# Kernel optimization log

Measured on AMD Instinct MI355X. Metric: run time of the kernel, lower is better.

## Reference

```python
import jax, jax.numpy as jnp
import numpy as np

NUM_HEADS = 16
DIM = 1024
HEAD_DIM = DIM // NUM_HEADS
SCALE = DIM ** (-0.5)  # note: module scales by dim_out**-0.5, not head_dim**-0.5
ROPE_THETA = 10000.0


def _rope_cos_sin(seq_len, head_dim, dtype):
    # lucidrains default: freqs = 1/theta^(arange(0,d,2)/d), interleaved-repeat to d
    inv_freq = 1.0 / (ROPE_THETA ** (np.arange(0, head_dim, 2, dtype=np.float32) / head_dim))
    t = np.arange(seq_len, dtype=np.float32)
    freqs = np.einsum('i,j->ij', t, inv_freq)            # [T, d/2]
    freqs = np.repeat(freqs, 2, axis=-1)                  # [T, d] interleaved repeat
    return jnp.asarray(np.cos(freqs), dtype), jnp.asarray(np.sin(freqs), dtype)


def _rotate_half(x):
    # interleaved pairs: (x1, x2) -> (-x2, x1)
    x1 = x[..., ::2]
    x2 = x[..., 1::2]
    return jnp.stack([-x2, x1], axis=-1).reshape(x.shape)


def _apply_rope(x, cos, sin):
    # x: [B, H, T, d]; cos/sin: [T, d]
    return x * cos + _rotate_half(x) * sin


def setup_inputs() -> dict:
    key = jax.random.key(0)
    ks = jax.random.split(key, 6)
    B, T = 4, 2048
    s = DIM ** -0.5
    return {
        'x':  jax.random.normal(ks[0], (B, T, DIM), jnp.float32),
        'h':  32,
        'w':  64,
        'Wq': jax.random.normal(ks[1], (DIM, DIM), jnp.float32) * s,
        'Wk': jax.random.normal(ks[2], (DIM, DIM), jnp.float32) * s,
        'Wv': jax.random.normal(ks[3], (DIM, DIM), jnp.float32) * s,
        'Wp': jax.random.normal(ks[4], (DIM, DIM), jnp.float32) * s,
        'bp': jax.random.normal(ks[5], (DIM,), jnp.float32) * 0.01,
    }


def reference(x, h, w, Wq, Wk, Wv, Wp, bp):
    B, T, _ = x.shape
    split = lambda y: y.reshape(B, T, NUM_HEADS, HEAD_DIM).transpose(0, 2, 1, 3)  # b h t d
    q = split(x @ Wq)
    k = split(x @ Wk)
    v = split(x @ Wv)
    cos, sin = _rope_cos_sin(T, HEAD_DIM, x.dtype)
    q = _apply_rope(q, cos, sin)
    k = _apply_rope(k, cos, sin)
    attn = jax.nn.softmax(jnp.einsum('bhld,bhtd->bhlt', q, k) * SCALE, axis=-1)
    out = jnp.einsum('bhlt,bhtd->bhld', attn, v)
    out = out.transpose(0, 2, 1, 3).reshape(B, T, DIM)  # b t (h d)
    return out @ Wp + bp
```

## Files before the change

kernel.cpp:

```cpp
#include <hip/hip_runtime.h>

typedef unsigned short u16;
typedef unsigned int u32;
typedef __attribute__((ext_vector_type(8))) short short8;
typedef __attribute__((ext_vector_type(4))) short short4v;
typedef __attribute__((ext_vector_type(4))) float f32x4;
typedef __attribute__((ext_vector_type(16))) float f32x16;

__device__ __forceinline__ u16 f2bf(float f) {
  u32 u = __float_as_uint(f);
  u = (u + 0x7fffu + ((u >> 16) & 1u)) >> 16;
  return (u16)u;
}
__device__ __forceinline__ float bf2f(u16 h) {
  return __uint_as_float(((u32)h) << 16);
}
__device__ __forceinline__ void glds16(const u16* g, u16* l) {
  __builtin_amdgcn_global_load_lds(
      (const __attribute__((address_space(1))) void*)g,
      (__attribute__((address_space(3))) void*)l, 16, 0, 0);
}

__global__ __launch_bounds__(256) void rope_tab_k(float* __restrict__ cosT,
                                                  float* __restrict__ sinT) {
  int idx = blockIdx.x * 256 + threadIdx.x;
  int t = idx >> 5, i = idx & 31;
  float inv = powf(10000.0f, -(float)i / 32.0f);
  float ang = (float)t * inv;
  float s, c;
  sincosf(ang, &s, &c);
  cosT[idx] = c;
  sinT[idx] = s;
}

__global__ __launch_bounds__(256) void cvt_x_k(const float* __restrict__ x,
                                               u16* __restrict__ xb) {
  int i = blockIdx.x * 256 + threadIdx.x;
  int e = i * 8;
  float4 a = *(const float4*)(x + e);
  float4 b = *(const float4*)(x + e + 4);
  short8 o;
  o[0] = (short)f2bf(a.x); o[1] = (short)f2bf(a.y);
  o[2] = (short)f2bf(a.z); o[3] = (short)f2bf(a.w);
  o[4] = (short)f2bf(b.x); o[5] = (short)f2bf(b.y);
  o[6] = (short)f2bf(b.z); o[7] = (short)f2bf(b.w);
  *(short8*)(xb + e) = o;
}

__global__ __launch_bounds__(256) void wtrans_k(const float* __restrict__ W0,
                                                const float* __restrict__ W1,
                                                const float* __restrict__ W2,
                                                const float* __restrict__ W3,
                                                u16* __restrict__ wt) {
  __shared__ float tl[64][65];
  const float* W = (blockIdx.z == 0) ? W0 : (blockIdx.z == 1) ? W1
                  : (blockIdx.z == 2) ? W2 : W3;
  u16* out = wt + (size_t)blockIdx.z * 1024 * 1024;
  int k0 = blockIdx.x * 64, n0 = blockIdx.y * 64;
  int tid = threadIdx.x;
  int rr = tid >> 4, cc4 = (tid & 15) * 4;
#pragma unroll
  for (int p = 0; p < 4; ++p) {
    int r = rr + p * 16;
    float4 v = *(const float4*)(W + (size_t)(k0 + r) * 1024 + n0 + cc4);
    tl[r][cc4] = v.x; tl[r][cc4 + 1] = v.y; tl[r][cc4 + 2] = v.z; tl[r][cc4 + 3] = v.w;
  }
  __syncthreads();
#pragma unroll
  for (int p = 0; p < 4; ++p) {
    int rn = rr + p * 16;
    short4v o;
    o[0] = (short)f2bf(tl[cc4][rn]);     o[1] = (short)f2bf(tl[cc4 + 1][rn]);
    o[2] = (short)f2bf(tl[cc4 + 2][rn]); o[3] = (short)f2bf(tl[cc4 + 3][rn]);
    *(short4v*)(out + (size_t)(n0 + rn) * 1024 + k0 + cc4) = o;
  }
}

__global__ __launch_bounds__(256) void gemm_qkv_k(const u16* __restrict__ xb,
                                                  const u16* __restrict__ wt,
                                                  u16* __restrict__ Qb,
                                                  u16* __restrict__ Kb,
                                                  u16* __restrict__ Vt) {
  __shared__ __align__(16) u16 Ash[128][32];
  __shared__ __align__(16) u16 Bsh[128][32];
  int tid = threadIdx.x;
  int lane = tid & 63, w = tid >> 6;
  int wr = w >> 1, wc = w & 1;
  int l15 = lane & 15, g = lane >> 4;
  int row0 = blockIdx.x * 128;
  int ncol0 = blockIdx.y * 128;

  f32x4 zero = {0.f, 0.f, 0.f, 0.f};
  f32x4 acc[4][4];
#pragma unroll
  for (int m = 0; m < 4; ++m)
#pragma unroll
    for (int n = 0; n < 4; ++n) acc[m][n] = zero;

  int aRow = tid >> 2, aK = (tid & 3) * 8;
  const u16* aSrc0 = xb + (size_t)(row0 + aRow) * 1024 + aK;
  const u16* aSrc1 = xb + (size_t)(row0 + 64 + aRow) * 1024 + aK;
  const u16* bSrc0 = wt + (size_t)(ncol0 + aRow) * 1024 + aK;
  const u16* bSrc1 = wt + (size_t)(ncol0 + 64 + aRow) * 1024 + aK;
  u16* ldsA0 = &Ash[0][0] + tid * 8;
  u16* ldsA1 = &Ash[0][0] + 2048 + tid * 8;
  u16* ldsB0 = &Bsh[0][0] + tid * 8;
  u16* ldsB1 = &Bsh[0][0] + 2048 + tid * 8;

  for (int kt = 0; kt < 32; ++kt) {
    __syncthreads();
    glds16(aSrc0, ldsA0); glds16(aSrc1, ldsA1);
    glds16(bSrc0, ldsB0); glds16(bSrc1, ldsB1);
    aSrc0 += 32; aSrc1 += 32; bSrc0 += 32; bSrc1 += 32;
    __syncthreads();
    short8 af[4], bfr[4];
#pragma unroll
    for (int m = 0; m < 4; ++m) af[m] = *(const short8*)&Ash[wr * 64 + m * 16 + l15][g * 8];
#pragma unroll
    for (int n = 0; n < 4; ++n) bfr[n] = *(const short8*)&Bsh[wc * 64 + n * 16 + l15][g * 8];
#pragma unroll
    for (int m = 0; m < 4; ++m)
#pragma unroll
      for (int n = 0; n < 4; ++n)
        acc[m][n] = __builtin_amdgcn_mfma_f32_16x16x32_bf16(af[m], bfr[n], acc[m][n], 0, 0, 0);
  }

  int c0 = ncol0 + wc * 64;
  int which = c0 >> 10;
  int rb = row0 + wr * 64;
#pragma unroll
  for (int m = 0; m < 4; ++m) {
    int r = rb + m * 16 + g * 4;
    int bb = r >> 11, t = r & 2047;
#pragma unroll
    for (int n = 0; n < 4; ++n) {
      int c = c0 + n * 16 + l15;
      int hh = (c & 1023) >> 6, d = c & 63;
      if (which == 2) {
        short4v o;
        o[0] = (short)f2bf(acc[m][n][0]); o[1] = (short)f2bf(acc[m][n][1]);
        o[2] = (short)f2bf(acc[m][n][2]); o[3] = (short)f2bf(acc[m][n][3]);
        *(short4v*)(Vt + ((size_t)((bb * 16 + hh) * 64 + d)) * 2048 + t) = o;
      } else {
        u16* dst = (which == 0 ? Qb : Kb) + ((size_t)((bb * 16 + hh) * 2048 + t)) * 64 + d;
        dst[0]   = f2bf(acc[m][n][0]);
        dst[64]  = f2bf(acc[m][n][1]);
        dst[128] = f2bf(acc[m][n][2]);
        dst[192] = f2bf(acc[m][n][3]);
      }
    }
  }
}

__global__ __launch_bounds__(256) void rope_k(u16* __restrict__ Qb, u16* __restrict__ Kb,
                                              const float* __restrict__ cosT,
                                              const float* __restrict__ sinT) {
  int i = blockIdx.x * 256 + threadIdx.x;
  u16* P; float sc; int j;
  if (i < 1048576) { P = Qb; sc = 0.03125f; j = i; }
  else             { P = Kb; sc = 1.0f;     j = i - 1048576; }
  int e = j * 8;
  int d0 = e & 63;
  int t = (e >> 6) & 2047;
  short8 v = *(const short8*)(P + e);
  const float* cb = cosT + t * 32 + (d0 >> 1);
  const float* sb = sinT + t * 32 + (d0 >> 1);
  short8 o;
#pragma unroll
  for (int p = 0; p < 4; ++p) {
    float c = cb[p], s = sb[p];
    float a = bf2f((u16)v[2 * p]), b = bf2f((u16)v[2 * p + 1]);
    o[2 * p]     = (short)f2bf((a * c - b * s) * sc);
    o[2 * p + 1] = (short)f2bf((b * c + a * s) * sc);
  }
  *(short8*)(P + e) = o;
}

__global__ __launch_bounds__(256) void attn_k(const u16* __restrict__ Q,
                                              const u16* __restrict__ K,
                                              const u16* __restrict__ Vt,
                                              u16* __restrict__ O) {
  __shared__ __align__(16) u16 KVs[2][2][4096];
  int bid = blockIdx.x;
  int head = (bid & 7) + ((bid >> 7) << 3);
  int qt = (bid >> 3) & 15;
  int bb = head >> 4, hh = head & 15;
  const u16* Qh = Q + (size_t)head * 131072;
  const u16* Kh = K + (size_t)head * 131072;
  const u16* Vh = Vt + (size_t)head * 131072;
  int tid = threadIdx.x, lane = tid & 63, w = tid >> 6;
  int l31 = lane & 31, hi = lane >> 5;
  int t0 = qt * 128 + w * 32;

  int srow = tid >> 3;
  int scol = ((tid & 7) ^ (srow & 7)) * 8;

  short8 qf[4];
#pragma unroll
  for (int ks = 0; ks < 4; ++ks)
    qf[ks] = *(const short8*)(Qh + (size_t)(t0 + l31) * 64 + ks * 16 + hi * 8);

  const u16* lds0 = &KVs[0][0][0];
  const u16* rpp[4];
#pragma unroll
  for (int j = 0; j < 4; ++j)
    rpp[j] = lds0 + l31 * 64 + ((((j * 2 + hi) ^ (lane & 7))) << 3);

  f32x16 zz;
#pragma unroll
  for (int i = 0; i < 16; ++i) zz[i] = 0.f;
  f32x16 oa0 = zz, oa1 = zz, oa2 = zz;
  short8 ones8 = {16256, 16256, 16256, 16256, 16256, 16256, 16256, 16256};

  const u16* kp = Kh + srow * 64 + scol;
  const u16* vp = Vh + srow * 2048 + scol;
  u16* sK = &KVs[0][0][0] + tid * 8;
  u16* sV = &KVs[0][1][0] + tid * 8;

#define STAGE_AT(BO) do {                                                      \
    glds16(kp,         sK + (BO));                                             \
    glds16(kp + 2048,  sK + (BO) + 2048);                                      \
    glds16(vp,         sV + (BO));                                             \
    glds16(vp + 65536, sV + (BO) + 2048);                                      \
    kp += 4096; vp += 64;                                                      \
  } while (0)

#define ATT_TILE(OB) do {                                                      \
    _Pragma("unroll")                                                          \
    for (int bl = 0; bl < 2; ++bl) {                                           \
      f32x16 pb = zz;                                                          \
      __builtin_amdgcn_s_setprio(1);                                           \
      _Pragma("unroll")                                                        \
      for (int ks = 0; ks < 4; ++ks) {                                         \
        short8 kf = *(const short8*)(rpp[ks] + (OB) + bl * 2048);              \
        pb = __builtin_amdgcn_mfma_f32_32x32x16_bf16(kf, qf[ks], pb, 0, 0, 0); \
      }                                                                        \
      __builtin_amdgcn_s_setprio(0);                                           \
      _Pragma("unroll")                                                        \
      for (int r = 0; r < 16; ++r) pb[r] = __expf(pb[r]);                      \
      u32 pk8[8];                                                              \
      _Pragma("unroll")                                                        \
      for (int j = 0; j < 8; ++j)                                              \
        asm("v_cvt_pk_bf16_f32 %0, %1, %2"                                     \
            : "=v"(pk8[j]) : "v"(pb[2 * j]), "v"(pb[2 * j + 1]));              \
      _Pragma("unroll")                                                        \
      for (int kb = 0; kb < 2; ++kb) {                                         \
        u32 w0 = pk8[4 * kb + 0], w2 = pk8[4 * kb + 2];                        \
        u32 w1 = pk8[4 * kb + 1], w3 = pk8[4 * kb + 3];                        \
        asm("v_permlane32_swap_b32 %0, %1" : "+v"(w0), "+v"(w2));              \
        asm("v_permlane32_swap_b32 %0, %1" : "+v"(w1), "+v"(w3));              \
        union { u32 u[4]; short8 s; } pu;                                      \
        pu.u[0] = w0; pu.u[1] = w1; pu.u[2] = w2; pu.u[3] = w3;                \
        const int kss = bl * 2 + kb;                                           \
        short8 vf0 = *(const short8*)(rpp[kss] + (OB) + 4096);                 \
        short8 vf1 = *(const short8*)(rpp[kss] + (OB) + 4096 + 2048);          \
        __builtin_amdgcn_s_setprio(1);                                         \
        oa0 = __builtin_amdgcn_mfma_f32_32x32x16_bf16(pu.s, vf0, oa0, 0,0,0);  \
        oa1 = __builtin_amdgcn_mfma_f32_32x32x16_bf16(pu.s, vf1, oa1, 0,0,0);  \
        oa2 = __builtin_amdgcn_mfma_f32_32x32x16_bf16(pu.s, ones8, oa2, 0,0,0);\
        __builtin_amdgcn_s_setprio(0);                                         \
      }                                                                        \
    }                                                                          \
  } while (0)

  STAGE_AT(0);
  for (int it = 0; it < 16; ++it) {
    STAGE_AT(8192);
    asm volatile("s_waitcnt vmcnt(4)\ns_barrier" ::: "memory");
    ATT_TILE(0);
    asm volatile("s_barrier" ::: "memory");
    if (it < 15) {
      STAGE_AT(0);
      asm volatile("s_waitcnt vmcnt(4)\ns_barrier" ::: "memory");
    } else {
      asm volatile("s_waitcnt vmcnt(0)\ns_barrier" ::: "memory");
    }
    ATT_TILE(8192);
    asm volatile("s_barrier" ::: "memory");
  }
#undef STAGE_AT
#undef ATT_TILE

  size_t obase = (size_t)(bb * 2048 + t0) * 1024 + hh * 64 + l31;
#pragma unroll
  for (int r = 0; r < 16; ++r) {
    int qr = (r & 3) + ((r >> 2) << 3) + (hi << 2);
    float ir = 1.0f / oa2[r];
    O[obase + (size_t)qr * 1024]      = f2bf(oa0[r] * ir);
    O[obase + (size_t)qr * 1024 + 32] = f2bf(oa1[r] * ir);
  }
}

__global__ __launch_bounds__(256) void gemm_out_k(const u16* __restrict__ Ob,
                                                  const u16* __restrict__ wt,
                                                  const float* __restrict__ bp,
                                                  float* __restrict__ out) {
  __shared__ __align__(16) u16 Ash[128][32];
  __shared__ __align__(16) u16 Bsh[128][32];
  int tid = threadIdx.x;
  int lane = tid & 63, w = tid >> 6;
  int wr = w >> 1, wc = w & 1;
  int l15 = lane & 15, g = lane >> 4;
  int row0 = blockIdx.x * 128;
  int ncol0 = blockIdx.y * 128;

  f32x4 zero = {0.f, 0.f, 0.f, 0.f};
  f32x4 acc[4][4];
#pragma unroll
  for (int m = 0; m < 4; ++m)
#pragma unroll
    for (int n = 0; n < 4; ++n) acc[m][n] = zero;

  int aRow = tid >> 2, aK = (tid & 3) * 8;
  const u16* aSrc0 = Ob + (size_t)(row0 + aRow) * 1024 + aK;
  const u16* aSrc1 = Ob + (size_t)(row0 + 64 + aRow) * 1024 + aK;
  const u16* bSrc0 = wt + (size_t)(ncol0 + aRow) * 1024 + aK;
  const u16* bSrc1 = wt + (size_t)(ncol0 + 64 + aRow) * 1024 + aK;
  u16* ldsA0 = &Ash[0][0] + tid * 8;
  u16* ldsA1 = &Ash[0][0] + 2048 + tid * 8;
  u16* ldsB0 = &Bsh[0][0] + tid * 8;
  u16* ldsB1 = &Bsh[0][0] + 2048 + tid * 8;

  for (int kt = 0; kt < 32; ++kt) {
    __syncthreads();
    glds16(aSrc0, ldsA0); glds16(aSrc1, ldsA1);
    glds16(bSrc0, ldsB0); glds16(bSrc1, ldsB1);
    aSrc0 += 32; aSrc1 += 32; bSrc0 += 32; bSrc1 += 32;
    __syncthreads();
    short8 af[4], bfr[4];
#pragma unroll
    for (int m = 0; m < 4; ++m) af[m] = *(const short8*)&Ash[wr * 64 + m * 16 + l15][g * 8];
#pragma unroll
    for (int n = 0; n < 4; ++n) bfr[n] = *(const short8*)&Bsh[wc * 64 + n * 16 + l15][g * 8];
#pragma unroll
    for (int m = 0; m < 4; ++m)
#pragma unroll
      for (int n = 0; n < 4; ++n)
        acc[m][n] = __builtin_amdgcn_mfma_f32_16x16x32_bf16(af[m], bfr[n], acc[m][n], 0, 0, 0);
  }

  int c0 = ncol0 + wc * 64;
  int rb = row0 + wr * 64;
  float bn[4];
#pragma unroll
  for (int n = 0; n < 4; ++n) bn[n] = bp[c0 + n * 16 + l15];
#pragma unroll
  for (int m = 0; m < 4; ++m) {
    int r = rb + m * 16 + g * 4;
#pragma unroll
    for (int n = 0; n < 4; ++n) {
      int c = c0 + n * 16 + l15;
      out[(size_t)(r + 0) * 1024 + c] = acc[m][n][0] + bn[n];
      out[(size_t)(r + 1) * 1024 + c] = acc[m][n][1] + bn[n];
      out[(size_t)(r + 2) * 1024 + c] = acc[m][n][2] + bn[n];
      out[(size_t)(r + 3) * 1024 + c] = acc[m][n][3] + bn[n];
    }
  }
}

extern "C" void kernel_launch(void* const* d_in, const int* in_sizes, int n_in,
                              void* d_out, int out_size, void* d_ws, size_t ws_size,
                              hipStream_t stream) {
  const float* x  = (const float*)d_in[0];
  const float* Wq = (const float*)d_in[3];
  const float* Wk = (const float*)d_in[4];
  const float* Wv = (const float*)d_in[5];
  const float* Wp = (const float*)d_in[6];
  const float* bp = (const float*)d_in[7];
  float* out = (float*)d_out;

  char* ws = (char*)d_ws;
  u16* xb   = (u16*)(ws);
  u16* wt   = (u16*)(ws + 16777216);
  u16* Qb   = (u16*)(ws + 25165824);
  u16* Kb   = (u16*)(ws + 41943040);
  u16* Vt   = (u16*)(ws + 58720256);
  u16* Ob   = (u16*)(ws + 75497472);
  float* cosT = (float*)(ws + 92274688);
  float* sinT = (float*)(ws + 92536832);

  rope_tab_k<<<256, 256, 0, stream>>>(cosT, sinT);
  cvt_x_k<<<4096, 256, 0, stream>>>(x, xb);
  dim3 tg(16, 16, 4);
  wtrans_k<<<tg, 256, 0, stream>>>(Wq, Wk, Wv, Wp, wt);
  dim3 g1(64, 24);
  gemm_qkv_k<<<g1, 256, 0, stream>>>(xb, wt, Qb, Kb, Vt);
  rope_k<<<8192, 256, 0, stream>>>(Qb, Kb, cosT, sinT);
  attn_k<<<1024, 256, 0, stream>>>(Qb, Kb, Vt, Ob);
  dim3 g2(64, 8);
  gemm_out_k<<<g2, 256, 0, stream>>>(Ob, wt + (size_t)3 * 1024 * 1024, bp, out);
}
```

Measured before the change: 208.8 us.

## Fuse RoPE into QKV GEMM epilogue and swizzle GEMM block order

The separate rope_k pass over Q and K is removed. RoPE rotation and the Q scale are now applied in the QKV GEMM epilogue, using a packed bf16 cos/sin table staged into LDS and a lane-xor shuffle to get the pair partner. Both GEMMs also remap block indices so that consecutive blocks share tiles, which should improve L2 reuse. In exchange the QKV kernel uses 16KB more LDS, and cos/sin are rounded to bf16, which slightly lowers precision.

```diff
diff --git a/kernel.cpp b/kernel.cpp
--- a/kernel.cpp
+++ b/kernel.cpp
@@ -21,16 +21,14 @@
       (__attribute__((address_space(3))) void*)l, 16, 0, 0);
 }
 
-__global__ __launch_bounds__(256) void rope_tab_k(float* __restrict__ cosT,
-                                                  float* __restrict__ sinT) {
+__global__ __launch_bounds__(256) void rope_tab_k(u32* __restrict__ cst) {
   int idx = blockIdx.x * 256 + threadIdx.x;
   int t = idx >> 5, i = idx & 31;
   float inv = powf(10000.0f, -(float)i / 32.0f);
   float ang = (float)t * inv;
   float s, c;
   sincosf(ang, &s, &c);
-  cosT[idx] = c;
-  sinT[idx] = s;
+  cst[idx] = (u32)f2bf(c) | ((u32)f2bf(s) << 16);
 }
 
 __global__ __launch_bounds__(256) void cvt_x_k(const float* __restrict__ x,
@@ -78,17 +76,31 @@
 
 __global__ __launch_bounds__(256) void gemm_qkv_k(const u16* __restrict__ xb,
                                                   const u16* __restrict__ wt,
+                                                  const u32* __restrict__ cst,
                                                   u16* __restrict__ Qb,
                                                   u16* __restrict__ Kb,
                                                   u16* __restrict__ Vt) {
   __shared__ __align__(16) u16 Ash[128][32];
   __shared__ __align__(16) u16 Bsh[128][32];
+  __shared__ __align__(16) u32 csl[4096];
   int tid = threadIdx.x;
   int lane = tid & 63, w = tid >> 6;
   int wr = w >> 1, wc = w & 1;
   int l15 = lane & 15, g = lane >> 4;
-  int row0 = blockIdx.x * 128;
-  int ncol0 = blockIdx.y * 128;
+
+  int lin = blockIdx.x + blockIdx.y * 64;
+  int sw = (lin & 7) * 192 + (lin >> 3);
+  int bx = sw & 63, by = sw >> 6;
+  int row0 = bx * 128;
+  int ncol0 = by * 128;
+  int which = by >> 3;
+
+  if (which < 2) {
+    const u16* src = (const u16*)(cst + (size_t)(row0 & 2047) * 32);
+#pragma unroll
+    for (int p = 0; p < 4; ++p)
+      glds16(src + p * 2048 + tid * 8, (u16*)csl + p * 2048 + tid * 8);
+  }
 
   f32x4 zero = {0.f, 0.f, 0.f, 0.f};
   f32x4 acc[4][4];
@@ -126,12 +138,14 @@
   }
 
   int c0 = ncol0 + wc * 64;
-  int which = c0 >> 10;
   int rb = row0 + wr * 64;
+  u32 sgnbit = (l15 & 1) ? 0u : 0x80000000u;
+  float qscale = (which == 0) ? 0.03125f : 1.0f;
 #pragma unroll
   for (int m = 0; m < 4; ++m) {
     int r = rb + m * 16 + g * 4;
     int bb = r >> 11, t = r & 2047;
+    int rowin = wr * 64 + m * 16 + g * 4;
 #pragma unroll
     for (int n = 0; n < 4; ++n) {
       int c = c0 + n * 16 + l15;
@@ -143,37 +157,21 @@
         *(short4v*)(Vt + ((size_t)((bb * 16 + hh) * 64 + d)) * 2048 + t) = o;
       } else {
         u16* dst = (which == 0 ? Qb : Kb) + ((size_t)((bb * 16 + hh) * 2048 + t)) * 64 + d;
-        dst[0]   = f2bf(acc[m][n][0]);
-        dst[64]  = f2bf(acc[m][n][1]);
-        dst[128] = f2bf(acc[m][n][2]);
-        dst[192] = f2bf(acc[m][n][3]);
+        int ci = (d >> 1);
+#pragma unroll
+        for (int j = 0; j < 4; ++j) {
+          float v = acc[m][n][j];
+          float p = __shfl_xor(v, 1);
+          u32 cs = csl[(rowin + j) * 32 + ci];
+          float c_ = __uint_as_float(cs << 16);
+          float s_ = __uint_as_float(cs & 0xffff0000u);
+          float ps = __uint_as_float(__float_as_uint(p * s_) ^ sgnbit);
+          float o = fmaf(v, c_, ps) * qscale;
+          dst[j * 64] = f2bf(o);
+        }
       }
     }
   }
-}
-
-__global__ __launch_bounds__(256) void rope_k(u16* __restrict__ Qb, u16* __restrict__ Kb,
-                                              const float* __restrict__ cosT,
-                                              const float* __restrict__ sinT) {
-  int i = blockIdx.x * 256 + threadIdx.x;
-  u16* P; float sc; int j;
-  if (i < 1048576) { P = Qb; sc = 0.03125f; j = i; }
-  else             { P = Kb; sc = 1.0f;     j = i - 1048576; }
-  int e = j * 8;
-  int d0 = e & 63;
-  int t = (e >> 6) & 2047;
-  short8 v = *(const short8*)(P + e);
-  const float* cb = cosT + t * 32 + (d0 >> 1);
-  const float* sb = sinT + t * 32 + (d0 >> 1);
-  short8 o;
-#pragma unroll
-  for (int p = 0; p < 4; ++p) {
-    float c = cb[p], s = sb[p];
-    float a = bf2f((u16)v[2 * p]), b = bf2f((u16)v[2 * p + 1]);
-    o[2 * p]     = (short)f2bf((a * c - b * s) * sc);
-    o[2 * p + 1] = (short)f2bf((b * c + a * s) * sc);
-  }
-  *(short8*)(P + e) = o;
 }
 
 __global__ __launch_bounds__(256) void attn_k(const u16* __restrict__ Q,
@@ -301,8 +299,12 @@
   int lane = tid & 63, w = tid >> 6;
   int wr = w >> 1, wc = w & 1;
   int l15 = lane & 15, g = lane >> 4;
-  int row0 = blockIdx.x * 128;
-  int ncol0 = blockIdx.y * 128;
+
+  int lin = blockIdx.x + blockIdx.y * 64;
+  int sw = (lin & 7) * 64 + (lin >> 3);
+  int bx = sw & 63, by = sw >> 6;
+  int row0 = bx * 128;
+  int ncol0 = by * 128;
 
   f32x4 zero = {0.f, 0.f, 0.f, 0.f};
   f32x4 acc[4][4];
@@ -376,16 +378,14 @@
   u16* Kb   = (u16*)(ws + 41943040);
   u16* Vt   = (u16*)(ws + 58720256);
   u16* Ob   = (u16*)(ws + 75497472);
-  float* cosT = (float*)(ws + 92274688);
-  float* sinT = (float*)(ws + 92536832);
-
-  rope_tab_k<<<256, 256, 0, stream>>>(cosT, sinT);
+  u32* cst  = (u32*)(ws + 92274688);
+
+  rope_tab_k<<<256, 256, 0, stream>>>(cst);
   cvt_x_k<<<4096, 256, 0, stream>>>(x, xb);
   dim3 tg(16, 16, 4);
   wtrans_k<<<tg, 256, 0, stream>>>(Wq, Wk, Wv, Wp, wt);
   dim3 g1(64, 24);
-  gemm_qkv_k<<<g1, 256, 0, stream>>>(xb, wt, Qb, Kb, Vt);
-  rope_k<<<8192, 256, 0, stream>>>(Qb, Kb, cosT, sinT);
+  gemm_qkv_k<<<g1, 256, 0, stream>>>(xb, wt, cst, Qb, Kb, Vt);
   attn_k<<<1024, 256, 0, stream>>>(Qb, Kb, Vt, Ob);
   dim3 g2(64, 8);
   gemm_out_k<<<g2, 256, 0, stream>>>(Ob, wt + (size_t)3 * 1024 * 1024, bp, out);
```

New measurement: 224.7 us. 7.6% more time.
